# Kernel optimization log

Measured on AMD Instinct MI355X. Metric: run time of the kernel, lower is better.

The kernel has to match this reference:

```python
import jax, jax.numpy as jnp
import numpy as np

B, S, F_IN = 8, 2048, 1024
H, SC = 512, 256
N_LAYERS = 3


def _glorot(key, shape):
    fan_in, fan_out = shape[-2], shape[-1]
    lim = float(np.sqrt(6.0 / (fan_in + fan_out)))
    return jax.random.uniform(key, shape, jnp.float32, -lim, lim)


def setup_inputs() -> dict:
    key = jax.random.key(0)
    ks = jax.random.split(key, 8)
    x = jax.random.normal(ks[0], (B, S, F_IN), jnp.float32)
    Wp = _glorot(ks[1], (F_IN, H)); bp = jnp.zeros((H,), jnp.float32)
    gcn_W = _glorot(ks[2], (N_LAYERS, H, H)); gcn_b = jnp.zeros((N_LAYERS, H), jnp.float32)
    s1_W = _glorot(ks[3], (H, SC)); s1_b = jnp.zeros((SC,), jnp.float32)
    s2_W = _glorot(ks[4], (SC, SC // 2)); s2_b = jnp.zeros((SC // 2,), jnp.float32)
    s3_W = _glorot(ks[5], (SC // 2, 1)); s3_b = jnp.zeros((1,), jnp.float32)
    return {"x": x, "Wp": Wp, "bp": bp, "gcn_W": gcn_W, "gcn_b": gcn_b,
            "s1_W": s1_W, "s1_b": s1_b, "s2_W": s2_W, "s2_b": s2_b,
            "s3_W": s3_W, "s3_b": s3_b}


def _build_adj(seq_len):
    # tridiagonal band: self + immediate temporal neighbors
    a = jnp.eye(seq_len, dtype=jnp.float32)
    a = a + jnp.eye(seq_len, k=1, dtype=jnp.float32) + jnp.eye(seq_len, k=-1, dtype=jnp.float32)
    deg = a.sum(axis=1)
    dinv = jnp.power(deg + 1e-8, -0.5)
    # D^{-1/2} A D^{-1/2}
    return dinv[:, None] * a * dinv[None, :]


def reference(x, Wp, bp, gcn_W, gcn_b, s1_W, s1_b, s2_W, s2_b, s3_W, s3_b):
    seq_len = x.shape[1]
    adj = _build_adj(seq_len)  # [S, S]
    h = jnp.einsum('bsf,fh->bsh', x, Wp) + bp  # feature projection
    for i in range(N_LAYERS):
        support = jnp.einsum('bsh,hk->bsk', h, gcn_W[i])
        h = jnp.einsum('st,btk->bsk', adj, support) + gcn_b[i]
        if i < N_LAYERS - 1:
            h = jax.nn.relu(h)  # dropout is identity in eval mode
    z = jax.nn.relu(jnp.einsum('bsh,hc->bsc', h, s1_W) + s1_b)
    z = jax.nn.relu(jnp.einsum('bsc,cd->bsd', z, s2_W) + s2_b)
    scores = jax.nn.sigmoid(jnp.einsum('bsd,do->bso', z, s3_W) + s3_b)
    return scores[..., 0]  # [B, S]
```

## Files before the change

### kernel.cpp

```cpp
#include <hip/hip_runtime.h>
#include <hip/hip_fp16.h>
#include <cstdint>
#include <cstddef>


typedef _Float16 f16;
typedef _Float16 f16x8 __attribute__((ext_vector_type(8)));
typedef float    f32x4 __attribute__((ext_vector_type(4)));

__device__ __forceinline__ void async_cp16(const void* g, void* l) {
  __builtin_amdgcn_global_load_lds((const __attribute__((address_space(1))) void*)g,
                                   (__attribute__((address_space(3))) void*)l, 16, 0, 0);
}

__device__ __forceinline__ f16x8 splat8(f16 v) {
  f16x8 r;
#pragma unroll
  for (int e = 0; e < 8; ++e) r[e] = v;
  return r;
}

template<int BM, int BN, bool RELU, bool HAS_BIAS>
__global__ __launch_bounds__(512, 4) void proj_gemm_kernel(
    const float* __restrict__ Aptr, const f16* __restrict__ BT,
    f16* __restrict__ C, const float* __restrict__ bias,
    int M, int N, int K)
{
  constexpr int BK = 64;
  constexpr int NT = 512;
  constexpr int WAVES_N = 4;
  constexpr int WM = BM / 2;
  constexpr int WN = BN / WAVES_N;
  constexpr int TM = WM / 16;
  constexpr int TN = WN / 16;
  constexpr int ITER_B = (BN * BK) / (NT * 8);

  __shared__ __align__(16) f16 sA[BM * BK];
  __shared__ __align__(16) f16 sB[BN * BK];

  const int tid  = threadIdx.x;
  const int lane = tid & 63;
  const int wave = tid >> 6;
  const int wm   = wave / WAVES_N;
  const int wn   = wave % WAVES_N;
  const int m0   = blockIdx.x * BM;
  const int n0   = blockIdx.y * BN;
  const int quad = lane >> 4;
  const int l16  = lane & 15;

  uint32_t offA;
  {
    const int row = tid >> 3;
    const int q   = (tid & 7) ^ (row & 7);
    offA = (uint32_t)(((size_t)(m0 + row) * K + q * 8) * 4);
  }

  f32x4 acc[TM][TN];
#pragma unroll
  for (int i = 0; i < TM; ++i)
#pragma unroll
    for (int j = 0; j < TN; ++j)
      acc[i][j] = (f32x4){0.f, 0.f, 0.f, 0.f};

  float4 pa0, pa1;
  {
    const float4* p = (const float4*)((const char*)Aptr + offA);
    pa0 = p[0]; pa1 = p[1];
  }

  for (int kt = 0; kt < K; kt += BK) {
#pragma unroll
    for (int j = 0; j < ITER_B; ++j) {
      const int linear = j * NT + tid;
      const int row = linear >> 3;
      const int q   = (linear & 7) ^ (row & 7);
      async_cp16(BT + (size_t)(n0 + row) * K + kt + q * 8, &sB[linear * 8]);
    }
    {
      f16x8 o;
      o[0] = (f16)pa0.x; o[1] = (f16)pa0.y; o[2] = (f16)pa0.z; o[3] = (f16)pa0.w;
      o[4] = (f16)pa1.x; o[5] = (f16)pa1.y; o[6] = (f16)pa1.z; o[7] = (f16)pa1.w;
      *(f16x8*)&sA[(size_t)tid * 8] = o;
    }
    __syncthreads();

    if (kt + BK < K) {
      const float4* p = (const float4*)((const char*)Aptr + (size_t)(kt + BK) * 4 + offA);
      pa0 = p[0]; pa1 = p[1];
    }

#pragma unroll
    for (int kk = 0; kk < 2; ++kk) {
      const int c = quad + kk * 4;
      f16x8 af[TM], bf[TN];
#pragma unroll
      for (int mi = 0; mi < TM; ++mi) {
        const int ml = wm * WM + mi * 16 + l16;
        af[mi] = *(const f16x8*)&sA[ml * 64 + ((c ^ (ml & 7)) * 8)];
      }
#pragma unroll
      for (int ni = 0; ni < TN; ++ni) {
        const int nl = wn * WN + ni * 16 + l16;
        bf[ni] = *(const f16x8*)&sB[nl * 64 + ((c ^ (nl & 7)) * 8)];
      }
#pragma unroll
      for (int mi = 0; mi < TM; ++mi)
#pragma unroll
        for (int ni = 0; ni < TN; ++ni)
          acc[mi][ni] = __builtin_amdgcn_mfma_f32_16x16x32_f16(
              af[mi], bf[ni], acc[mi][ni], 0, 0, 0);
    }
    __syncthreads();
  }

#pragma unroll
  for (int ni = 0; ni < TN; ++ni) {
    const int nc = n0 + wn * WN + ni * 16 + l16;
    const float bv = HAS_BIAS ? bias[nc] : 0.0f;
#pragma unroll
    for (int mi = 0; mi < TM; ++mi) {
#pragma unroll
      for (int r = 0; r < 4; ++r) {
        const int mr = m0 + wm * WM + mi * 16 + quad * 4 + r;
        float v = acc[mi][ni][r] + bv;
        if (RELU) v = fmaxf(v, 0.0f);
        C[(size_t)mr * N + nc] = (f16)v;
      }
    }
  }
}

template<bool RELU>
__global__ __launch_bounds__(256, 2) void gcn_gemm_kernel(
    const f16* __restrict__ hin, const f16* __restrict__ WT,
    f16* __restrict__ C, const float* __restrict__ bias, int M)
{
  constexpr int BM = 128, BN = 128, BK = 64;
  constexpr int NT = 256;
  constexpr int TM = 4, TN = 4;
  constexpr int S = 2048, H = 512;
  constexpr int AROWS = BM + 2;

  __shared__ __align__(16) f16 sA[AROWS * BK];
  __shared__ __align__(16) f16 sB[BN * BK];

  const int tid  = threadIdx.x;
  const int lane = tid & 63;
  const int wave = tid >> 6;
  const int wm   = wave >> 1;
  const int wn   = wave & 1;
  const int quad = lane >> 4;
  const int l16  = lane & 15;
  const int m0   = blockIdx.x * BM;
  const int n0   = blockIdx.y * BN;

  const float dM = 0.57735026919f;
  const float dE = 0.70710678118f;

  f16 cf[TM][3];
#pragma unroll
  for (int mi = 0; mi < TM; ++mi) {
    const int grow = m0 + wm * 64 + mi * 16 + l16;
    const int s = grow & (S - 1);
    const float dsv = (s == 0 || s == S - 1) ? dE : dM;
    cf[mi][0] = (f16)((s > 0)     ? dsv * ((s - 1 == 0) ? dE : dM)     : 0.0f);
    cf[mi][1] = (f16)(dsv * dsv);
    cf[mi][2] = (f16)((s < S - 1) ? dsv * ((s + 1 == S - 1) ? dE : dM) : 0.0f);
  }

  f32x4 acc[TM][TN];
#pragma unroll
  for (int i = 0; i < TM; ++i)
#pragma unroll
    for (int j = 0; j < TN; ++j)
      acc[i][j] = (f32x4){0.f, 0.f, 0.f, 0.f};

  for (int kt = 0; kt < H; kt += BK) {
#pragma unroll
    for (int j = 0; j < 4; ++j) {
      const int linear = j * NT + tid;
      const int row = linear >> 3;
      const int q   = (linear & 7) ^ (row & 7);
      async_cp16(WT + (size_t)(n0 + row) * H + kt + q * 8, &sB[linear * 8]);
    }
#pragma unroll
    for (int j = 0; j < 4; ++j) {
      const int chunk = j * NT + tid + 8;
      const int row = chunk >> 3;
      const int q   = (chunk & 7) ^ (row & 7);
      async_cp16(hin + (size_t)(m0 + row - 1) * H + kt + q * 8, &sA[chunk * 8]);
    }
    if (tid < 16) {
      const int hi = tid >> 3;
      const int ldsrow = hi ? (BM + 1) : 0;
      const int i = tid & 7;
      const int q = i ^ (ldsrow & 7);
      int g = m0 - 1 + ldsrow;
      g = g < 0 ? 0 : (g >= M ? M - 1 : g);
      f16x8 v = *(const f16x8*)(hin + (size_t)g * H + kt + q * 8);
      *(f16x8*)&sA[(size_t)(ldsrow * 8 + i) * 8] = v;
    }
    __syncthreads();

#pragma unroll
    for (int kk = 0; kk < 2; ++kk) {
      const int c = quad + kk * 4;
      f16x8 af[TM], bf[TN];
#pragma unroll
      for (int mi = 0; mi < TM; ++mi) {
        const int ldr = wm * 64 + mi * 16 + l16 + 1;
        f16x8 pv = *(const f16x8*)&sA[(ldr - 1) * 64 + ((c ^ ((ldr - 1) & 7)) * 8)];
        f16x8 sv = *(const f16x8*)&sA[(ldr    ) * 64 + ((c ^ ((ldr    ) & 7)) * 8)];
        f16x8 nv = *(const f16x8*)&sA[(ldr + 1) * 64 + ((c ^ ((ldr + 1) & 7)) * 8)];
        f16x8 r = pv * splat8(cf[mi][0]);
        r += sv * splat8(cf[mi][1]);
        r += nv * splat8(cf[mi][2]);
        af[mi] = r;
      }
#pragma unroll
      for (int ni = 0; ni < TN; ++ni) {
        const int nl = wn * 64 + ni * 16 + l16;
        bf[ni] = *(const f16x8*)&sB[nl * 64 + ((c ^ (nl & 7)) * 8)];
      }
#pragma unroll
      for (int mi = 0; mi < TM; ++mi)
#pragma unroll
        for (int ni = 0; ni < TN; ++ni)
          acc[mi][ni] = __builtin_amdgcn_mfma_f32_16x16x32_f16(
              af[mi], bf[ni], acc[mi][ni], 0, 0, 0);
    }
    __syncthreads();
  }

#pragma unroll
  for (int ni = 0; ni < TN; ++ni) {
    const int nc = n0 + wn * 64 + ni * 16 + l16;
    const float bv = bias[nc];
#pragma unroll
    for (int mi = 0; mi < TM; ++mi) {
#pragma unroll
      for (int r = 0; r < 4; ++r) {
        const int mr = m0 + wm * 64 + mi * 16 + quad * 4 + r;
        float v = acc[mi][ni][r] + bv;
        if (RELU) v = fmaxf(v, 0.0f);
        C[(size_t)mr * H + nc] = (f16)v;
      }
    }
  }
}

__global__ __launch_bounds__(256) void head_fused_kernel(
    const f16* __restrict__ h, const f16* __restrict__ S1T,
    const f16* __restrict__ S2T,
    const float* __restrict__ s1b, const float* __restrict__ s2b,
    const float* __restrict__ s3w, const float* __restrict__ s3b,
    float* __restrict__ out)
{
  __shared__ __align__(16) char smem[36864 + 32 * 264 * 2];
  f16* sA  = (f16*)smem;
  f16* sB  = (f16*)(smem + 4096);
  f16* zs  = (f16*)(smem + 36864);
  f16* z2s = (f16*)smem;
  f16* sB2 = (f16*)(smem + 8704);

  const int tid  = threadIdx.x;
  const int lane = tid & 63;
  const int wave = tid >> 6;
  const int quad = lane >> 4;
  const int l16  = lane & 15;
  const int m0   = blockIdx.x * 32;

  f32x4 acc[2][4];
#pragma unroll
  for (int i = 0; i < 2; ++i)
#pragma unroll
    for (int j = 0; j < 4; ++j) acc[i][j] = (f32x4){0.f, 0.f, 0.f, 0.f};

  for (int kt = 0; kt < 512; kt += 64) {
    __syncthreads();
    {
      const int linear = tid;
      const int row = linear >> 3;
      const int q   = (linear & 7) ^ (row & 7);
      async_cp16(h + (size_t)(m0 + row) * 512 + kt + q * 8, &sA[linear * 8]);
    }
#pragma unroll
    for (int j = 0; j < 8; ++j) {
      const int linear = j * 256 + tid;
      const int row = linear >> 3;
      const int q   = (linear & 7) ^ (row & 7);
      async_cp16(S1T + (size_t)row * 512 + kt + q * 8, &sB[linear * 8]);
    }
    __syncthreads();
#pragma unroll
    for (int kk = 0; kk < 2; ++kk) {
      const int c = quad + kk * 4;
      f16x8 af[2], bf[4];
#pragma unroll
      for (int mi = 0; mi < 2; ++mi) {
        const int ml = mi * 16 + l16;
        af[mi] = *(const f16x8*)&sA[ml * 64 + ((c ^ (ml & 7)) * 8)];
      }
#pragma unroll
      for (int ni = 0; ni < 4; ++ni) {
        const int nl = wave * 64 + ni * 16 + l16;
        bf[ni] = *(const f16x8*)&sB[nl * 64 + ((c ^ (nl & 7)) * 8)];
      }
#pragma unroll
      for (int mi = 0; mi < 2; ++mi)
#pragma unroll
        for (int ni = 0; ni < 4; ++ni)
          acc[mi][ni] = __builtin_amdgcn_mfma_f32_16x16x32_f16(
              af[mi], bf[ni], acc[mi][ni], 0, 0, 0);
    }
  }
#pragma unroll
  for (int ni = 0; ni < 4; ++ni) {
    const int nc = wave * 64 + ni * 16 + l16;
    const float bv = s1b[nc];
#pragma unroll
    for (int mi = 0; mi < 2; ++mi)
#pragma unroll
      for (int r = 0; r < 4; ++r) {
        const int row = mi * 16 + quad * 4 + r;
        zs[row * 264 + nc] = (f16)fmaxf(acc[mi][ni][r] + bv, 0.0f);
      }
  }
  __syncthreads();

  f32x4 acc2[2][2];
#pragma unroll
  for (int i = 0; i < 2; ++i)
#pragma unroll
    for (int j = 0; j < 2; ++j) acc2[i][j] = (f32x4){0.f, 0.f, 0.f, 0.f};

  for (int kt2 = 0; kt2 < 4; ++kt2) {
    __syncthreads();
#pragma unroll
    for (int j = 0; j < 4; ++j) {
      const int linear = j * 256 + tid;
      const int row = linear >> 3;
      const int q   = (linear & 7) ^ (row & 7);
      async_cp16(S2T + (size_t)row * 256 + kt2 * 64 + q * 8, &sB2[linear * 8]);
    }
    __syncthreads();
#pragma unroll
    for (int kk = 0; kk < 2; ++kk) {
      const int c = quad + kk * 4;
      f16x8 af[2], bf[2];
#pragma unroll
      for (int mi = 0; mi < 2; ++mi) {
        const int row = mi * 16 + l16;
        af[mi] = *(const f16x8*)&zs[row * 264 + (kt2 * 8 + c) * 8];
      }
#pragma unroll
      for (int ni = 0; ni < 2; ++ni) {
        const int nl = wave * 32 + ni * 16 + l16;
        bf[ni] = *(const f16x8*)&sB2[nl * 64 + ((c ^ (nl & 7)) * 8)];
      }
#pragma unroll
      for (int mi = 0; mi < 2; ++mi)
#pragma unroll
        for (int ni = 0; ni < 2; ++ni)
          acc2[mi][ni] = __builtin_amdgcn_mfma_f32_16x16x32_f16(
              af[mi], bf[ni], acc2[mi][ni], 0, 0, 0);
    }
  }
  __syncthreads();
#pragma unroll
  for (int ni = 0; ni < 2; ++ni) {
    const int nc = wave * 32 + ni * 16 + l16;
    const float bv = s2b[nc];
#pragma unroll
    for (int mi = 0; mi < 2; ++mi)
#pragma unroll
      for (int r = 0; r < 4; ++r) {
        const int row = mi * 16 + quad * 4 + r;
        z2s[row * 136 + nc] = (f16)fmaxf(acc2[mi][ni][r] + bv, 0.0f);
      }
  }
  __syncthreads();

  const int m  = tid >> 3;
  const int qd = tid & 7;
  float p = 0.f;
#pragma unroll
  for (int j = 0; j < 2; ++j) {
    f16x8 v = *(const f16x8*)&z2s[m * 136 + qd * 16 + j * 8];
#pragma unroll
    for (int e = 0; e < 8; ++e) p += (float)v[e] * s3w[qd * 16 + j * 8 + e];
  }
  p += __shfl_xor(p, 1);
  p += __shfl_xor(p, 2);
  p += __shfl_xor(p, 4);
  if (qd == 0) out[m0 + m] = 1.0f / (1.0f + expf(-(p + s3b[0])));
}

__global__ __launch_bounds__(256) void prep_kernel(
    const float* __restrict__ Wp, f16* __restrict__ WpT,
    const float* __restrict__ gW, f16* __restrict__ GT,
    const float* __restrict__ s1W, f16* __restrict__ S1T,
    const float* __restrict__ s2W, f16* __restrict__ S2T)
{
  __shared__ f16 s[64 * 68];
  const int tid = threadIdx.x;
  int b = blockIdx.x;

  const float* W; f16* WT; int K, N, tile;
  if (b < 128)      { W = Wp;  WT = WpT; K = 1024; N = 512; tile = b; }
  else if (b < 320) { const int i = (b - 128) >> 6;
                      W = gW + (size_t)i * 262144; WT = GT + (size_t)i * 262144;
                      K = 512; N = 512; tile = (b - 128) & 63; }
  else if (b < 352) { W = s1W; WT = S1T; K = 512; N = 256; tile = b - 320; }
  else              { W = s2W; WT = S2T; K = 256; N = 128; tile = b - 352; }

  const int nt = tile % (N >> 6);
  const int kt = tile / (N >> 6);
#pragma unroll
  for (int it = 0; it < 16; ++it) {
    const int i  = it * 256 + tid;
    const int rk = i >> 6, rn = i & 63;
    s[rn * 68 + rk] = (f16)W[(size_t)(kt * 64 + rk) * N + nt * 64 + rn];
  }
  __syncthreads();
#pragma unroll
  for (int it = 0; it < 16; ++it) {
    const int i  = it * 256 + tid;
    const int rn = i >> 6, rk = i & 63;
    WT[(size_t)(nt * 64 + rn) * K + kt * 64 + rk] = s[rn * 68 + rk];
  }
}

extern "C" void kernel_launch(void* const* d_in, const int* in_sizes, int n_in,
                              void* d_out, int out_size, void* d_ws, size_t ws_size,
                              hipStream_t stream) {
  (void)in_sizes; (void)n_in; (void)out_size; (void)ws_size;
  const float* x   = (const float*)d_in[0];
  const float* Wp  = (const float*)d_in[1];
  const float* bp  = (const float*)d_in[2];
  const float* gW  = (const float*)d_in[3];
  const float* gb  = (const float*)d_in[4];
  const float* s1W = (const float*)d_in[5];
  const float* s1b = (const float*)d_in[6];
  const float* s2W = (const float*)d_in[7];
  const float* s2b = (const float*)d_in[8];
  const float* s3W = (const float*)d_in[9];
  const float* s3b = (const float*)d_in[10];
  float* out = (float*)d_out;

  constexpr int M = 16384;
  char* ws = (char*)d_ws;
  f16* hA  = (f16*)(ws + 0);
  f16* hB  = (f16*)(ws + 16777216);
  f16* WpT = (f16*)(ws + 33554432);
  f16* GT  = (f16*)(ws + 34603008);
  f16* S1T = (f16*)(ws + 36175872);
  f16* S2T = (f16*)(ws + 36438016);

  prep_kernel<<<360, 256, 0, stream>>>(Wp, WpT, gW, GT, s1W, S1T, s2W, S2T);

  proj_gemm_kernel<64, 256, false, true>
      <<<dim3(M / 64, 2), 512, 0, stream>>>(x, WpT, hA, bp, M, 512, 1024);

  gcn_gemm_kernel<true>
      <<<dim3(M / 128, 4), 256, 0, stream>>>(hA, GT, hB, gb, M);
  gcn_gemm_kernel<true>
      <<<dim3(M / 128, 4), 256, 0, stream>>>(hB, GT + 262144, hA, gb + 512, M);
  gcn_gemm_kernel<false>
      <<<dim3(M / 128, 4), 256, 0, stream>>>(hA, GT + 524288, hB, gb + 1024, M);

  head_fused_kernel<<<M / 32, 256, 0, stream>>>(hB, S1T, S2T, s1b, s2b, s3W, s3b, out);
}
```

Baseline: 199.6 us.

## Double-buffer LDS tiles in projection and GCN GEMM kernels

Both the projection GEMM and the GCN GEMM now use two LDS buffers per operand. The next K tile is prefetched with async global-to-LDS copies (plus register staging for the fp32 A tile and the halo rows) while MFMAs run on the current buffer, which drops one barrier per iteration. This is meant to hide global load latency behind compute, at the cost of twice the shared memory. To allow for that, the projection kernel's launch-bounds occupancy hint goes from 4 to 2.

```diff
diff --git a/kernel.cpp b/kernel.cpp
--- a/kernel.cpp
+++ b/kernel.cpp
@@ -21,7 +21,7 @@
 }
 
 template<int BM, int BN, bool RELU, bool HAS_BIAS>
-__global__ __launch_bounds__(512, 4) void proj_gemm_kernel(
+__global__ __launch_bounds__(512, 2) void proj_gemm_kernel(
     const float* __restrict__ Aptr, const f16* __restrict__ BT,
     f16* __restrict__ C, const float* __restrict__ bias,
     int M, int N, int K)
@@ -35,8 +35,8 @@
   constexpr int TN = WN / 16;
   constexpr int ITER_B = (BN * BK) / (NT * 8);
 
-  __shared__ __align__(16) f16 sA[BM * BK];
-  __shared__ __align__(16) f16 sB[BN * BK];
+  __shared__ __align__(16) f16 sA[2][BM * BK];
+  __shared__ __align__(16) f16 sB[2][BN * BK];
 
   const int tid  = threadIdx.x;
   const int lane = tid & 63;
@@ -63,32 +63,23 @@
       acc[i][j] = (f32x4){0.f, 0.f, 0.f, 0.f};
 
   float4 pa0, pa1;
-  {
-    const float4* p = (const float4*)((const char*)Aptr + offA);
-    pa0 = p[0]; pa1 = p[1];
-  }
-
-  for (int kt = 0; kt < K; kt += BK) {
+
+  auto stageB = [&](int kt, int b) {
 #pragma unroll
     for (int j = 0; j < ITER_B; ++j) {
       const int linear = j * NT + tid;
       const int row = linear >> 3;
       const int q   = (linear & 7) ^ (row & 7);
-      async_cp16(BT + (size_t)(n0 + row) * K + kt + q * 8, &sB[linear * 8]);
-    }
-    {
-      f16x8 o;
-      o[0] = (f16)pa0.x; o[1] = (f16)pa0.y; o[2] = (f16)pa0.z; o[3] = (f16)pa0.w;
-      o[4] = (f16)pa1.x; o[5] = (f16)pa1.y; o[6] = (f16)pa1.z; o[7] = (f16)pa1.w;
-      *(f16x8*)&sA[(size_t)tid * 8] = o;
-    }
-    __syncthreads();
-
-    if (kt + BK < K) {
-      const float4* p = (const float4*)((const char*)Aptr + (size_t)(kt + BK) * 4 + offA);
-      pa0 = p[0]; pa1 = p[1];
-    }
-
+      async_cp16(BT + (size_t)(n0 + row) * K + kt + q * 8, &sB[b][linear * 8]);
+    }
+  };
+  auto writeA = [&](int b) {
+    f16x8 o;
+    o[0] = (f16)pa0.x; o[1] = (f16)pa0.y; o[2] = (f16)pa0.z; o[3] = (f16)pa0.w;
+    o[4] = (f16)pa1.x; o[5] = (f16)pa1.y; o[6] = (f16)pa1.z; o[7] = (f16)pa1.w;
+    *(f16x8*)&sA[b][(size_t)tid * 8] = o;
+  };
+  auto compute = [&](int b) {
 #pragma unroll
     for (int kk = 0; kk < 2; ++kk) {
       const int c = quad + kk * 4;
@@ -96,12 +87,12 @@
 #pragma unroll
       for (int mi = 0; mi < TM; ++mi) {
         const int ml = wm * WM + mi * 16 + l16;
-        af[mi] = *(const f16x8*)&sA[ml * 64 + ((c ^ (ml & 7)) * 8)];
+        af[mi] = *(const f16x8*)&sA[b][ml * 64 + ((c ^ (ml & 7)) * 8)];
       }
 #pragma unroll
       for (int ni = 0; ni < TN; ++ni) {
         const int nl = wn * WN + ni * 16 + l16;
-        bf[ni] = *(const f16x8*)&sB[nl * 64 + ((c ^ (nl & 7)) * 8)];
+        bf[ni] = *(const f16x8*)&sB[b][nl * 64 + ((c ^ (nl & 7)) * 8)];
       }
 #pragma unroll
       for (int mi = 0; mi < TM; ++mi)
@@ -110,6 +101,27 @@
           acc[mi][ni] = __builtin_amdgcn_mfma_f32_16x16x32_f16(
               af[mi], bf[ni], acc[mi][ni], 0, 0, 0);
     }
+  };
+
+  {
+    const float4* p = (const float4*)((const char*)Aptr + offA);
+    pa0 = p[0]; pa1 = p[1];
+  }
+  stageB(0, 0);
+  writeA(0);
+  __syncthreads();
+
+  const int nt = K / BK;
+  for (int t = 0; t < nt; ++t) {
+    const int cur = t & 1;
+    const bool pf = (t + 1 < nt);
+    if (pf) {
+      const float4* p = (const float4*)((const char*)Aptr + (size_t)(t + 1) * BK * 4 + offA);
+      pa0 = p[0]; pa1 = p[1];
+      stageB((t + 1) * BK, cur ^ 1);
+    }
+    compute(cur);
+    if (pf) writeA(cur ^ 1);
     __syncthreads();
   }
 
@@ -141,8 +153,8 @@
   constexpr int S = 2048, H = 512;
   constexpr int AROWS = BM + 2;
 
-  __shared__ __align__(16) f16 sA[AROWS * BK];
-  __shared__ __align__(16) f16 sB[BN * BK];
+  __shared__ __align__(16) f16 sA[2][AROWS * BK];
+  __shared__ __align__(16) f16 sB[2][BN * BK];
 
   const int tid  = threadIdx.x;
   const int lane = tid & 63;
@@ -168,40 +180,44 @@
     cf[mi][2] = (f16)((s < S - 1) ? dsv * ((s + 1 == S - 1) ? dE : dM) : 0.0f);
   }
 
-  f32x4 acc[TM][TN];
-#pragma unroll
-  for (int i = 0; i < TM; ++i)
-#pragma unroll
-    for (int j = 0; j < TN; ++j)
-      acc[i][j] = (f32x4){0.f, 0.f, 0.f, 0.f};
-
-  for (int kt = 0; kt < H; kt += BK) {
+  const int h_row = (tid >> 3) ? (BM + 1) : 0;
+  const int h_i   = tid & 7;
+  const int h_q   = h_i ^ (h_row & 7);
+  int hg = m0 - 1 + h_row;
+  hg = hg < 0 ? 0 : (hg >= M ? M - 1 : hg);
+  f16x8 h_v;
+
+  auto halo_load = [&](int kt) {
+    if (tid < 16) h_v = *(const f16x8*)(hin + (size_t)hg * H + kt + h_q * 8);
+  };
+  auto halo_write = [&](int b) {
+    if (tid < 16) *(f16x8*)&sA[b][(size_t)(h_row * 8 + h_i) * 8] = h_v;
+  };
+  auto stage_glds = [&](int kt, int b) {
 #pragma unroll
     for (int j = 0; j < 4; ++j) {
       const int linear = j * NT + tid;
       const int row = linear >> 3;
       const int q   = (linear & 7) ^ (row & 7);
-      async_cp16(WT + (size_t)(n0 + row) * H + kt + q * 8, &sB[linear * 8]);
+      async_cp16(WT + (size_t)(n0 + row) * H + kt + q * 8, &sB[b][linear * 8]);
     }
 #pragma unroll
     for (int j = 0; j < 4; ++j) {
       const int chunk = j * NT + tid + 8;
       const int row = chunk >> 3;
       const int q   = (chunk & 7) ^ (row & 7);
-      async_cp16(hin + (size_t)(m0 + row - 1) * H + kt + q * 8, &sA[chunk * 8]);
-    }
-    if (tid < 16) {
-      const int hi = tid >> 3;
-      const int ldsrow = hi ? (BM + 1) : 0;
-      const int i = tid & 7;
-      const int q = i ^ (ldsrow & 7);
-      int g = m0 - 1 + ldsrow;
-      g = g < 0 ? 0 : (g >= M ? M - 1 : g);
-      f16x8 v = *(const f16x8*)(hin + (size_t)g * H + kt + q * 8);
-      *(f16x8*)&sA[(size_t)(ldsrow * 8 + i) * 8] = v;
-    }
-    __syncthreads();
-
+      async_cp16(hin + (size_t)(m0 + row - 1) * H + kt + q * 8, &sA[b][chunk * 8]);
+    }
+  };
+
+  f32x4 acc[TM][TN];
+#pragma unroll
+  for (int i = 0; i < TM; ++i)
+#pragma unroll
+    for (int j = 0; j < TN; ++j)
+      acc[i][j] = (f32x4){0.f, 0.f, 0.f, 0.f};
+
+  auto compute = [&](int b) {
 #pragma unroll
     for (int kk = 0; kk < 2; ++kk) {
       const int c = quad + kk * 4;
@@ -209,9 +225,9 @@
 #pragma unroll
       for (int mi = 0; mi < TM; ++mi) {
         const int ldr = wm * 64 + mi * 16 + l16 + 1;
-        f16x8 pv = *(const f16x8*)&sA[(ldr - 1) * 64 + ((c ^ ((ldr - 1) & 7)) * 8)];
-        f16x8 sv = *(const f16x8*)&sA[(ldr    ) * 64 + ((c ^ ((ldr    ) & 7)) * 8)];
-        f16x8 nv = *(const f16x8*)&sA[(ldr + 1) * 64 + ((c ^ ((ldr + 1) & 7)) * 8)];
+        f16x8 pv = *(const f16x8*)&sA[b][(ldr - 1) * 64 + ((c ^ ((ldr - 1) & 7)) * 8)];
+        f16x8 sv = *(const f16x8*)&sA[b][(ldr    ) * 64 + ((c ^ ((ldr    ) & 7)) * 8)];
+        f16x8 nv = *(const f16x8*)&sA[b][(ldr + 1) * 64 + ((c ^ ((ldr + 1) & 7)) * 8)];
         f16x8 r = pv * splat8(cf[mi][0]);
         r += sv * splat8(cf[mi][1]);
         r += nv * splat8(cf[mi][2]);
@@ -220,7 +236,7 @@
 #pragma unroll
       for (int ni = 0; ni < TN; ++ni) {
         const int nl = wn * 64 + ni * 16 + l16;
-        bf[ni] = *(const f16x8*)&sB[nl * 64 + ((c ^ (nl & 7)) * 8)];
+        bf[ni] = *(const f16x8*)&sB[b][nl * 64 + ((c ^ (nl & 7)) * 8)];
       }
 #pragma unroll
       for (int mi = 0; mi < TM; ++mi)
@@ -229,6 +245,23 @@
           acc[mi][ni] = __builtin_amdgcn_mfma_f32_16x16x32_f16(
               af[mi], bf[ni], acc[mi][ni], 0, 0, 0);
     }
+  };
+
+  halo_load(0);
+  stage_glds(0, 0);
+  halo_write(0);
+  __syncthreads();
+
+  constexpr int NTILES = H / BK;
+  for (int t = 0; t < NTILES; ++t) {
+    const int cur = t & 1;
+    const bool pf = (t + 1 < NTILES);
+    if (pf) {
+      halo_load((t + 1) * BK);
+      stage_glds((t + 1) * BK, cur ^ 1);
+    }
+    compute(cur);
+    if (pf) halo_write(cur ^ 1);
     __syncthreads();
   }
 
```

Result: no change. 198.6 us (-0.5%).
